# Kernel optimization log

Measured on AMD Instinct MI355X. Metric: run time of the kernel, lower is better.

Reference implementation:

```python
import jax, jax.numpy as jnp
import numpy as np
from math import factorial

# ---- static config mirroring Cace.__init__ ----
MAX_L = 3            # max angular degree
N_RBF = 8            # Bessel radial basis size
RB = 8               # n_radial_basis (radial embedding dim after transform)
K = 3                # n_atom_basis -> edge channels C = K*K
NZ = 4               # len(zs)
CUTOFF = 5.5
N_NODES = 2000
N_EDGES = 50000
T_MP = 1             # num_message_passing
MP_NORM = 1.0 / np.sqrt(25.0)   # 1/sqrt(avg_num_neighbors)
C = K * K

def _lxlylz(max_l):
    out = []
    for l in range(max_l + 1):
        for lx in range(l, -1, -1):
            for ly in range(l - lx, -1, -1):
                out.append((lx, ly, l - lx - ly))
    return out

L_LIST = _lxlylz(MAX_L)                 # 20 Cartesian monomials for max_l=3
NL = len(L_LIST)
LX = np.array([t[0] for t in L_LIST]); LY = np.array([t[1] for t in L_LIST]); LZ = np.array([t[2] for t in L_LIST])
DEGS = LX + LY + LZ                     # degree l of each monomial
MULTI = np.array([factorial(int(d)) / (factorial(int(a)) * factorial(int(b)) * factorial(int(c)))
                  for a, b, c, d in zip(LX, LY, LZ, DEGS)], dtype=np.float32)
SEL = np.zeros((NL, MAX_L + 1), np.float32)
SEL[np.arange(NL), DEGS] = 1.0          # monomial -> degree one-hot (for per-l sums)
NB = 1 + (MAX_L + 1)                    # symmetrizer feats: nu=1 (l=0) + nu=2 per l

def bessel(r):  # [E] -> [E, N_RBF]
    n = jnp.arange(1, N_RBF + 1, dtype=r.dtype)
    return jnp.sqrt(2.0 / CUTOFF) * jnp.sin(n[None, :] * jnp.pi * r[:, None] / CUTOFF) / r[:, None]

def poly_cutoff(r):  # MACE-style polynomial cutoff, p=6
    p = 6.0
    u = r / CUTOFF
    f = 1.0 - (p + 1.0) * (p + 2.0) / 2.0 * u**6 + p * (p + 2.0) * u**7 - p * (p + 1.0) / 2.0 * u**8
    return f * (u < 1.0)

def axis_pows(x):  # [E] -> [E, MAX_L+1] = x^0..x^MAX_L (safe grads, handles negatives)
    pows = [jnp.ones_like(x)]
    for _ in range(MAX_L):
        pows.append(pows[-1] * x)
    return jnp.stack(pows, axis=1)

def angular(u):  # unit vectors [E,3] -> Cartesian monomials [E, NL]
    return axis_pows(u[:, 0])[:, LX] * axis_pows(u[:, 1])[:, LY] * axis_pows(u[:, 2])[:, LZ]

def radial_transform(x, W):  # x [N,R,L,C], W [MAX_L+1,R,Rb] shared per degree l
    return jnp.einsum('nrlc,lrb->nblc', x, W[DEGS])

def symmetrize(A):  # A [N,Rb,NL,C] -> B [N,Rb,NB,C]
    b1 = A[:, :, :1, :]  # nu=1: the (0,0,0) monomial (index 0)
    w = (A * A) * jnp.asarray(MULTI)[None, None, :, None]
    b2 = jnp.einsum('nrlc,lm->nrmc', w, jnp.asarray(SEL))  # nu=2 invariant per degree l
    return jnp.concatenate([b1, b2], axis=2)


def setup_inputs() -> dict:
    key = jax.random.key(0)
    ks = jax.random.split(key, 9)
    positions = jax.random.uniform(ks[0], (N_NODES, 3), dtype=jnp.float32) * 12.0
    species = jax.random.randint(ks[1], (N_NODES,), 0, NZ)
    send = jax.random.randint(ks[2], (N_EDGES,), 0, N_NODES)
    off = jax.random.randint(ks[3], (N_EDGES,), 1, N_NODES)
    recv = (send + off) % N_NODES  # no self-edges -> strictly positive edge lengths
    edge_index = jnp.stack([send, recv])
    shifts = jnp.zeros((N_EDGES, 3), jnp.float32)
    W_embed = jax.random.normal(ks[4], (NZ, K), jnp.float32)
    W_radial = jax.random.normal(ks[5], (MAX_L + 1, N_RBF, RB), jnp.float32) / np.sqrt(N_RBF)
    W_mem = jax.random.normal(ks[6], (MAX_L + 1, RB, RB), jnp.float32) / np.sqrt(RB)
    W_ar = jax.random.normal(ks[7], (N_RBF, RB), jnp.float32) / np.sqrt(N_RBF)
    W_chi = jax.random.normal(ks[8], (RB, NB), jnp.float32) * 0.1
    return {"positions": positions, "shifts": shifts, "W_embed": W_embed, "W_radial": W_radial,
            "W_mem": W_mem, "W_ar": W_ar, "W_chi": W_chi, "species": species, "edge_index": edge_index}


def reference(positions, shifts, W_embed, W_radial, W_mem, W_ar, W_chi, species, edge_index):
    n_nodes = positions.shape[0]
    send, recv = edge_index[0], edge_index[1]
    # edge geometry
    vec = positions[recv] - positions[send] + shifts
    lengths = jnp.linalg.norm(vec, axis=-1)
    u = vec / (lengths[:, None] + 1e-9)
    rad = bessel(lengths)          # [E,R]
    fcut = poly_cutoff(lengths)    # [E]
    ang = angular(u)               # [E,NL]
    # edge type encoding: outer product of sender/receiver species embeddings
    emb = W_embed[species]         # [N,K]
    enc = (emb[send][:, :, None] * emb[recv][:, None, :]).reshape(-1, C)  # [E,C]
    # elementwise_multiply_3tensors -> [E,R,NL,C]
    edge_attri = jnp.einsum('er,el,ec->erlc', rad * fcut[:, None], ang, enc)
    A = radial_transform(jax.ops.segment_sum(edge_attri, recv, num_segments=n_nodes), W_radial)  # [N,Rb,NL,C]
    B = symmetrize(A)              # [N,Rb,NB,C]
    feats = [B]
    for _ in range(T_MP):
        mem = jnp.einsum('nrlc,lrb->nblc', A, W_mem[DEGS])        # NodeMemory
        chi = jnp.einsum('nbkc,bk->nc', B, W_chi)                  # MessageBchi node scalar
        msg_bchi = edge_attri * chi[send][:, None, None, :]
        A_bchi = radial_transform(jax.ops.segment_sum(msg_bchi, recv, num_segments=n_nodes), W_radial)
        fr = (rad @ W_ar) * fcut[:, None]                          # MessageAr radial filter [E,Rb]
        msg_ar = A[send] * fr[:, :, None, None]
        A_ar = jax.ops.segment_sum(msg_ar, recv, num_segments=n_nodes)
        A = (A_ar + A_bchi) * MP_NORM + mem
        B = symmetrize(A)
        feats.append(B)
    return jnp.stack(feats, axis=-1)   # [N,Rb,NB,C,T_MP+1]
```

## Files before the change

kernel.cpp:

```cpp
#include <hip/hip_runtime.h>
#include <hip/hip_bf16.h>


#define CUTF 5.5f
#define MPNORM 0.2f

__constant__ int   d_DEGS[20]  = {0,1,1,1,2,2,2,2,2,2,3,3,3,3,3,3,3,3,3,3};
__constant__ float d_MULTI[20] = {1,1,1,1,1,2,2,1,2,1,1,3,3,3,6,3,1,3,3,1};

__global__ __launch_bounds__(1024) void k_prep(const int* __restrict__ eidx,
                                               int* __restrict__ offs,
                                               int* __restrict__ cursor,
                                               int N, int E) {
  __shared__ int cnt[2048];
  __shared__ int part[1024];
  int t = threadIdx.x;
  cnt[t] = 0; cnt[t + 1024] = 0;
  for (int i = t; i < N; i += 1024) cursor[i] = 0;
  __syncthreads();
  const int* recv = eidx + E;
  if ((E & 3) == 0) {
    #pragma unroll 2
    for (int i = t * 4; i + 3 < E; i += 4096) {
      int4 v = *reinterpret_cast<const int4*>(recv + i);
      atomicAdd(&cnt[v.x], 1); atomicAdd(&cnt[v.y], 1);
      atomicAdd(&cnt[v.z], 1); atomicAdd(&cnt[v.w], 1);
    }
  } else {
    #pragma unroll 4
    for (int i = t; i < E; i += 1024) atomicAdd(&cnt[recv[i]], 1);
  }
  __syncthreads();
  int a = cnt[2 * t], b = cnt[2 * t + 1];
  int s = a + b;
  part[t] = s;
  __syncthreads();
  for (int d = 1; d < 1024; d <<= 1) {
    int add = (t >= d) ? part[t - d] : 0;
    __syncthreads();
    part[t] += add;
    __syncthreads();
  }
  int excl = part[t] - s;
  if (2 * t     < N) offs[2 * t]     = excl;
  if (2 * t + 1 < N) offs[2 * t + 1] = excl + a;
  if (t == 1023) offs[N] = part[1023];
}

__global__ void k_edge(const float* __restrict__ pos,
                       const float* __restrict__ shifts,
                       const float* __restrict__ Wemb,
                       const float* __restrict__ War,
                       const int* __restrict__ species,
                       const int* __restrict__ eidx,
                       const int* __restrict__ offs,
                       int* __restrict__ cursor,
                       float* __restrict__ edata,
                       int* __restrict__ esend,
                       int E) {
  __shared__ float war_s[64];
  int t = threadIdx.x;
  if (t < 64) war_s[t] = War[t];
  __syncthreads();
  int e = blockIdx.x * blockDim.x + t;
  if (e >= E) return;
  int s  = eidx[e];
  int rI = eidx[E + e];
  float vx = pos[rI*3+0] - pos[s*3+0] + shifts[e*3+0];
  float vy = pos[rI*3+1] - pos[s*3+1] + shifts[e*3+1];
  float vz = pos[rI*3+2] - pos[s*3+2] + shifts[e*3+2];
  float len = sqrtf(vx*vx + vy*vy + vz*vz);
  float inv = 1.0f / (len + 1e-9f);
  float ux = vx*inv, uy = vy*inv, uz = vz*inv;
  float uu = len * (1.0f/CUTF);
  float u2 = uu*uu, u6 = u2*u2*u2;
  float fcut = (uu < 1.0f) ? (1.0f - 28.0f*u6 + 48.0f*u6*uu - 21.0f*u6*u2) : 0.0f;
  float x = 3.14159265358979f * uu;
  float sn = sinf(x), c2 = 2.0f*cosf(x), snm1 = 0.0f;
  float pref = sqrtf(2.0f/CUTF) / (len + 1e-20f);
  float rad[8];
  float v[48];
  #pragma unroll
  for (int k = 0; k < 8; k++) {
    rad[k] = pref * sn;
    v[k]   = rad[k] * fcut;
    float nxt = c2*sn - snm1; snm1 = sn; sn = nxt;
  }
  #pragma unroll
  for (int b = 0; b < 8; b++) {
    float a = 0.0f;
    #pragma unroll
    for (int k = 0; k < 8; k++) a += rad[k] * war_s[k*8+b];
    v[8+b] = a * fcut;
  }
  float px2 = ux*ux, py2 = uy*uy, pz2 = uz*uz;
  v[16] = 1.0f; v[17] = ux;     v[18] = uy;     v[19] = uz;
  v[20] = px2;  v[21] = ux*uy;  v[22] = ux*uz;  v[23] = py2;
  v[24] = uy*uz;v[25] = pz2;
  v[26] = px2*ux; v[27] = px2*uy; v[28] = px2*uz; v[29] = ux*py2;
  v[30] = ux*uy*uz; v[31] = ux*pz2; v[32] = py2*uy; v[33] = py2*uz;
  v[34] = uy*pz2; v[35] = pz2*uz;
  int zs = species[s], zr = species[rI];
  float es0 = Wemb[zs*3+0], es1 = Wemb[zs*3+1], es2 = Wemb[zs*3+2];
  float er0 = Wemb[zr*3+0], er1 = Wemb[zr*3+1], er2 = Wemb[zr*3+2];
  v[36] = es0*er0; v[37] = es0*er1; v[38] = es0*er2;
  v[39] = es1*er0; v[40] = es1*er1; v[41] = es1*er2;
  v[42] = es2*er0; v[43] = es2*er1; v[44] = es2*er2;
  v[45] = 0.0f; v[46] = 0.0f; v[47] = 0.0f;
  int slot = atomicAdd(&cursor[rI], 1);
  int dst = offs[rI] + slot;
  float4* eb4 = reinterpret_cast<float4*>(edata + (size_t)dst * 48);
  #pragma unroll
  for (int w = 0; w < 12; w++)
    eb4[w] = make_float4(v[4*w], v[4*w+1], v[4*w+2], v[4*w+3]);
  esend[dst] = s;
}

__global__ __launch_bounds__(192) void k_nodeA(
    const float* __restrict__ edata, const int* __restrict__ offs,
    const float* __restrict__ Wrad, const float* __restrict__ Wchi,
    float* __restrict__ A, uint4* __restrict__ Abf2,
    float* __restrict__ chi, float* __restrict__ B0, int N) {
  __shared__ float wr_s[288];
  __shared__ float wchi_s[40];
  __shared__ float Bsh[360];
  int t = threadIdx.x, n = blockIdx.x;
  for (int i = t; i < 256; i += 192) { int d = i >> 6, rm = i & 63; wr_s[d*72+rm] = Wrad[i]; }
  for (int i = t; i < 40;  i += 192) wchi_s[i] = Wchi[i];
  for (int i = t; i < 360; i += 192) Bsh[i] = 0.0f;
  int l = t / 9, c = t - l*9;
  bool act = t < 180;
  int ll = act ? l : 0, cc = act ? c : 0;
  float acc[8];
  #pragma unroll
  for (int r = 0; r < 8; r++) acc[r] = 0.0f;
  int start = offs[n], end = offs[n+1];
  #pragma unroll 4
  for (int j = start; j < end; j++) {
    const float* row = edata + (size_t)j * 48;
    float p = row[16+ll] * row[36+cc];
    #pragma unroll
    for (int r = 0; r < 8; r++) acc[r] += row[r] * p;
  }
  __syncthreads();
  int deg = act ? d_DEGS[ll] : 0;
  const float* wp = &wr_s[deg*72];
  float Ab[8];
  #pragma unroll
  for (int b = 0; b < 8; b++) {
    float a = 0.0f;
    #pragma unroll
    for (int r = 0; r < 8; r++) a += acc[r] * wp[r*8+b];
    Ab[b] = a;
  }
  if (act) {
    #pragma unroll
    for (int b = 0; b < 8; b++) A[(size_t)n*1440 + t*8 + b] = Ab[b];
    unsigned int pk[4];
    #pragma unroll
    for (int bp = 0; bp < 4; bp++) {
      __hip_bfloat16 blo = __float2bfloat16(Ab[2*bp]);
      __hip_bfloat16 bhi = __float2bfloat16(Ab[2*bp+1]);
      pk[bp] = (unsigned int)(*reinterpret_cast<unsigned short*>(&blo))
             | ((unsigned int)(*reinterpret_cast<unsigned short*>(&bhi)) << 16);
    }
    uint4 q; q.x = pk[0]; q.y = pk[1]; q.z = pk[2]; q.w = pk[3];
    Abf2[(size_t)n*180 + t] = q;
    if (l == 0) {
      #pragma unroll
      for (int b = 0; b < 8; b++) Bsh[b*45 + c] = Ab[b];
    }
    float mlt = d_MULTI[ll]; int kk = 1 + deg;
    #pragma unroll
    for (int b = 0; b < 8; b++) atomicAdd(&Bsh[b*45 + kk*9 + c], mlt*Ab[b]*Ab[b]);
  }
  __syncthreads();
  if (t < 9) {
    float s = 0.0f;
    for (int b = 0; b < 8; b++)
      #pragma unroll
      for (int kq = 0; kq < 5; kq++) s += Bsh[b*45 + kq*9 + t] * wchi_s[b*5 + kq];
    chi[n*9 + t] = s;
  }
  for (int i = t; i < 360; i += 192)
    B0[(size_t)n*360 + i] = Bsh[i];
}

__global__ __launch_bounds__(192) void k_node2(
    const float* __restrict__ edata, const int* __restrict__ esend,
    const int* __restrict__ offs,
    const float* __restrict__ Wrad, const float* __restrict__ Wmem,
    const float* __restrict__ A, const uint4* __restrict__ Abf2,
    const float* __restrict__ chi, const float* __restrict__ B0,
    float* __restrict__ out, int N) {
  __shared__ float wr_s[288], wm_s[288];
  __shared__ float Bsh[360];
  int t = threadIdx.x, n = blockIdx.x;
  for (int i = t; i < 256; i += 192) {
    int d = i >> 6, rm = i & 63;
    wr_s[d*72+rm] = Wrad[i];
    wm_s[d*72+rm] = Wmem[i];
  }
  for (int i = t; i < 360; i += 192) Bsh[i] = 0.0f;
  int l = t / 9, c = t - l*9;
  bool act = t < 180;
  int ll = act ? l : 0, cc = act ? c : 0;
  int tt = act ? t : 0;
  float Sacc[8], ARacc[8];
  #pragma unroll
  for (int r = 0; r < 8; r++) { Sacc[r] = 0.0f; ARacc[r] = 0.0f; }
  int start = offs[n], end = offs[n+1];
  #pragma unroll 4
  for (int j = start; j < end; j++) {
    const float* row = edata + (size_t)j * 48;
    int snd = esend[j];
    float ch = chi[snd*9 + cc];
    float pch = row[16+ll] * row[36+cc] * ch;
    #pragma unroll
    for (int r = 0; r < 8; r++) Sacc[r] += row[r] * pch;
    const uint4 q = Abf2[(size_t)snd*180 + tt];
    float a0 = __uint_as_float(q.x << 16), a1 = __uint_as_float(q.x & 0xffff0000u);
    float a2 = __uint_as_float(q.y << 16), a3 = __uint_as_float(q.y & 0xffff0000u);
    float a4 = __uint_as_float(q.z << 16), a5 = __uint_as_float(q.z & 0xffff0000u);
    float a6 = __uint_as_float(q.w << 16), a7 = __uint_as_float(q.w & 0xffff0000u);
    ARacc[0] += a0*row[8];  ARacc[1] += a1*row[9];
    ARacc[2] += a2*row[10]; ARacc[3] += a3*row[11];
    ARacc[4] += a4*row[12]; ARacc[5] += a5*row[13];
    ARacc[6] += a6*row[14]; ARacc[7] += a7*row[15];
  }
  __syncthreads();
  if (act) {
    int deg = d_DEGS[ll];
    const float* wrp = &wr_s[deg*72];
    const float* wmp = &wm_s[deg*72];
    const float* aop = A + (size_t)n*1440 + t*8;
    float aown[8];
    #pragma unroll
    for (int r = 0; r < 8; r++) aown[r] = aop[r];
    float newA[8];
    #pragma unroll
    for (int b = 0; b < 8; b++) {
      float mem = 0.0f, ab = 0.0f;
      #pragma unroll
      for (int r = 0; r < 8; r++) { mem += aown[r]*wmp[r*8+b]; ab += Sacc[r]*wrp[r*8+b]; }
      newA[b] = (ARacc[b] + ab)*MPNORM + mem;
    }
    if (l == 0) {
      #pragma unroll
      for (int b = 0; b < 8; b++) Bsh[b*45 + c] = newA[b];
    }
    float mlt = d_MULTI[ll]; int kk = 1 + deg;
    #pragma unroll
    for (int b = 0; b < 8; b++) atomicAdd(&Bsh[b*45 + kk*9 + c], mlt*newA[b]*newA[b]);
  }
  __syncthreads();
  float2* out2 = reinterpret_cast<float2*>(out);
  for (int i = t; i < 360; i += 192) {
    float2 pk; pk.x = B0[(size_t)n*360 + i]; pk.y = Bsh[i];
    out2[(size_t)n*360 + i] = pk;
  }
}

extern "C" void kernel_launch(void* const* d_in, const int* in_sizes, int n_in,
                              void* d_out, int out_size, void* d_ws, size_t ws_size,
                              hipStream_t stream) {
  const float* pos    = (const float*)d_in[0];
  const float* shifts = (const float*)d_in[1];
  const float* Wemb   = (const float*)d_in[2];
  const float* Wrad   = (const float*)d_in[3];
  const float* Wmem   = (const float*)d_in[4];
  const float* War    = (const float*)d_in[5];
  const float* Wchi   = (const float*)d_in[6];
  const int* species = (const int*)d_in[7];
  const int* eidx    = (const int*)d_in[8];
  float* out = (float*)d_out;
  int N = in_sizes[7];
  int E = in_sizes[8] / 2;

  char* base = (char*)d_ws;
  size_t off = 0;
  float* edata = (float*)(base + off); off += (size_t)E*48*4;
  float* A     = (float*)(base + off); off += (size_t)N*1440*4;
  uint4* Abf2  = (uint4*)(base + off); off += (size_t)N*180*16;
  float* chi   = (float*)(base + off); off += (size_t)N*9*4;
  float* B0    = (float*)(base + off); off += (size_t)N*360*4;
  int* cursor  = (int*)(base + off);   off += (size_t)N*4;
  int* offs    = (int*)(base + off);   off += (((size_t)(N+1)*4) + 15) & ~(size_t)15;
  int* esend   = (int*)(base + off);   off += (size_t)E*4;

  int eb = (E + 255) / 256;
  k_prep<<<1, 1024, 0, stream>>>(eidx, offs, cursor, N, E);
  k_edge<<<eb, 256, 0, stream>>>(pos, shifts, Wemb, War, species, eidx, offs, cursor,
                                 edata, esend, E);
  k_nodeA<<<N, 192, 0, stream>>>(edata, offs, Wrad, Wchi, A, Abf2, chi, B0, N);
  k_node2<<<N, 192, 0, stream>>>(edata, esend, offs, Wrad, Wmem, A, Abf2, chi, B0, out, N);
}
```

Measured before the change: 151.8 us.

## Fuse edge feature computation into node kernels and recompute instead of materializing

Removes the separate edge kernel and its 48-float-per-edge buffer. k_prep now builds a sorted edge permutation (eorig) from the atomic ranks, and each node kernel recomputes edge features for its incoming edges in shared-memory chunks. k_node2 recomputes the first-layer A accumulation and B0 instead of reading A and B0 from global memory. This trades extra recomputation (trig, geometry) and an extra single-block scatter pass in k_prep for less global memory traffic and one fewer launch.

```diff
diff --git a/kernel.cpp b/kernel.cpp
--- a/kernel.cpp
+++ b/kernel.cpp
@@ -4,31 +4,34 @@
 
 #define CUTF 5.5f
 #define MPNORM 0.2f
+#define RSTR 52
+#define CHUNK 64
 
 __constant__ int   d_DEGS[20]  = {0,1,1,1,2,2,2,2,2,2,3,3,3,3,3,3,3,3,3,3};
 __constant__ float d_MULTI[20] = {1,1,1,1,1,2,2,1,2,1,1,3,3,3,6,3,1,3,3,1};
 
 __global__ __launch_bounds__(1024) void k_prep(const int* __restrict__ eidx,
                                                int* __restrict__ offs,
-                                               int* __restrict__ cursor,
+                                               int* __restrict__ erank,
+                                               int* __restrict__ eorig,
                                                int N, int E) {
   __shared__ int cnt[2048];
   __shared__ int part[1024];
   int t = threadIdx.x;
   cnt[t] = 0; cnt[t + 1024] = 0;
-  for (int i = t; i < N; i += 1024) cursor[i] = 0;
   __syncthreads();
   const int* recv = eidx + E;
   if ((E & 3) == 0) {
-    #pragma unroll 2
     for (int i = t * 4; i + 3 < E; i += 4096) {
       int4 v = *reinterpret_cast<const int4*>(recv + i);
-      atomicAdd(&cnt[v.x], 1); atomicAdd(&cnt[v.y], 1);
-      atomicAdd(&cnt[v.z], 1); atomicAdd(&cnt[v.w], 1);
+      int r0 = atomicAdd(&cnt[v.x], 1);
+      int r1 = atomicAdd(&cnt[v.y], 1);
+      int r2 = atomicAdd(&cnt[v.z], 1);
+      int r3 = atomicAdd(&cnt[v.w], 1);
+      *reinterpret_cast<int4*>(erank + i) = make_int4(r0, r1, r2, r3);
     }
   } else {
-    #pragma unroll 4
-    for (int i = t; i < E; i += 1024) atomicAdd(&cnt[recv[i]], 1);
+    for (int i = t; i < E; i += 1024) erank[i] = atomicAdd(&cnt[recv[i]], 1);
   }
   __syncthreads();
   int a = cnt[2 * t], b = cnt[2 * t + 1];
@@ -45,30 +48,27 @@
   if (2 * t     < N) offs[2 * t]     = excl;
   if (2 * t + 1 < N) offs[2 * t + 1] = excl + a;
   if (t == 1023) offs[N] = part[1023];
-}
-
-__global__ void k_edge(const float* __restrict__ pos,
-                       const float* __restrict__ shifts,
-                       const float* __restrict__ Wemb,
-                       const float* __restrict__ War,
-                       const int* __restrict__ species,
-                       const int* __restrict__ eidx,
-                       const int* __restrict__ offs,
-                       int* __restrict__ cursor,
-                       float* __restrict__ edata,
-                       int* __restrict__ esend,
-                       int E) {
-  __shared__ float war_s[64];
-  int t = threadIdx.x;
-  if (t < 64) war_s[t] = War[t];
-  __syncthreads();
-  int e = blockIdx.x * blockDim.x + t;
-  if (e >= E) return;
-  int s  = eidx[e];
-  int rI = eidx[E + e];
-  float vx = pos[rI*3+0] - pos[s*3+0] + shifts[e*3+0];
-  float vy = pos[rI*3+1] - pos[s*3+1] + shifts[e*3+1];
-  float vz = pos[rI*3+2] - pos[s*3+2] + shifts[e*3+2];
+  cnt[2 * t] = excl;
+  cnt[2 * t + 1] = excl + a;
+  __syncthreads();
+  for (int i = t; i < E; i += 1024) {
+    int r = recv[i];
+    eorig[cnt[r] + erank[i]] = i;
+  }
+}
+
+template <bool WANT_FR>
+__device__ __forceinline__ void edge_feats(
+    int e, int n,
+    const float* __restrict__ pos, const float* __restrict__ shifts,
+    const float* __restrict__ Wemb, const int* __restrict__ species,
+    const int* __restrict__ eidx,
+    const float* war_s, float* row, int* snd_slot) {
+  int s = eidx[e];
+  *snd_slot = s;
+  float vx = pos[n*3+0] - pos[s*3+0] + shifts[e*3+0];
+  float vy = pos[n*3+1] - pos[s*3+1] + shifts[e*3+1];
+  float vz = pos[n*3+2] - pos[s*3+2] + shifts[e*3+2];
   float len = sqrtf(vx*vx + vy*vy + vz*vz);
   float inv = 1.0f / (len + 1e-9f);
   float ux = vx*inv, uy = vy*inv, uz = vz*inv;
@@ -79,48 +79,45 @@
   float sn = sinf(x), c2 = 2.0f*cosf(x), snm1 = 0.0f;
   float pref = sqrtf(2.0f/CUTF) / (len + 1e-20f);
   float rad[8];
-  float v[48];
   #pragma unroll
   for (int k = 0; k < 8; k++) {
     rad[k] = pref * sn;
-    v[k]   = rad[k] * fcut;
+    row[k] = rad[k] * fcut;
     float nxt = c2*sn - snm1; snm1 = sn; sn = nxt;
   }
-  #pragma unroll
-  for (int b = 0; b < 8; b++) {
-    float a = 0.0f;
-    #pragma unroll
-    for (int k = 0; k < 8; k++) a += rad[k] * war_s[k*8+b];
-    v[8+b] = a * fcut;
+  if (WANT_FR) {
+    #pragma unroll
+    for (int b = 0; b < 8; b++) {
+      float a = 0.0f;
+      #pragma unroll
+      for (int k = 0; k < 8; k++) a += rad[k] * war_s[k*8+b];
+      row[8+b] = a * fcut;
+    }
   }
   float px2 = ux*ux, py2 = uy*uy, pz2 = uz*uz;
-  v[16] = 1.0f; v[17] = ux;     v[18] = uy;     v[19] = uz;
-  v[20] = px2;  v[21] = ux*uy;  v[22] = ux*uz;  v[23] = py2;
-  v[24] = uy*uz;v[25] = pz2;
-  v[26] = px2*ux; v[27] = px2*uy; v[28] = px2*uz; v[29] = ux*py2;
-  v[30] = ux*uy*uz; v[31] = ux*pz2; v[32] = py2*uy; v[33] = py2*uz;
-  v[34] = uy*pz2; v[35] = pz2*uz;
-  int zs = species[s], zr = species[rI];
+  row[16] = 1.0f;   row[17] = ux;     row[18] = uy;     row[19] = uz;
+  row[20] = px2;    row[21] = ux*uy;  row[22] = ux*uz;  row[23] = py2;
+  row[24] = uy*uz;  row[25] = pz2;
+  row[26] = px2*ux; row[27] = px2*uy; row[28] = px2*uz; row[29] = ux*py2;
+  row[30] = ux*uy*uz; row[31] = ux*pz2; row[32] = py2*uy; row[33] = py2*uz;
+  row[34] = uy*pz2; row[35] = pz2*uz;
+  int zs = species[s], zr = species[n];
   float es0 = Wemb[zs*3+0], es1 = Wemb[zs*3+1], es2 = Wemb[zs*3+2];
   float er0 = Wemb[zr*3+0], er1 = Wemb[zr*3+1], er2 = Wemb[zr*3+2];
-  v[36] = es0*er0; v[37] = es0*er1; v[38] = es0*er2;
-  v[39] = es1*er0; v[40] = es1*er1; v[41] = es1*er2;
-  v[42] = es2*er0; v[43] = es2*er1; v[44] = es2*er2;
-  v[45] = 0.0f; v[46] = 0.0f; v[47] = 0.0f;
-  int slot = atomicAdd(&cursor[rI], 1);
-  int dst = offs[rI] + slot;
-  float4* eb4 = reinterpret_cast<float4*>(edata + (size_t)dst * 48);
-  #pragma unroll
-  for (int w = 0; w < 12; w++)
-    eb4[w] = make_float4(v[4*w], v[4*w+1], v[4*w+2], v[4*w+3]);
-  esend[dst] = s;
+  row[36] = es0*er0; row[37] = es0*er1; row[38] = es0*er2;
+  row[39] = es1*er0; row[40] = es1*er1; row[41] = es1*er2;
+  row[42] = es2*er0; row[43] = es2*er1; row[44] = es2*er2;
 }
 
 __global__ __launch_bounds__(192) void k_nodeA(
-    const float* __restrict__ edata, const int* __restrict__ offs,
+    const float* __restrict__ pos, const float* __restrict__ shifts,
+    const float* __restrict__ Wemb, const int* __restrict__ species,
+    const int* __restrict__ eidx, const int* __restrict__ eorig,
+    const int* __restrict__ offs,
     const float* __restrict__ Wrad, const float* __restrict__ Wchi,
-    float* __restrict__ A, uint4* __restrict__ Abf2,
-    float* __restrict__ chi, float* __restrict__ B0, int N) {
+    uint4* __restrict__ Abf2, float* __restrict__ chi, int N) {
+  __shared__ __align__(16) float srow[CHUNK * RSTR];
+  __shared__ int ssnd[CHUNK];
   __shared__ float wr_s[288];
   __shared__ float wchi_s[40];
   __shared__ float Bsh[360];
@@ -134,17 +131,29 @@
   float acc[8];
   #pragma unroll
   for (int r = 0; r < 8; r++) acc[r] = 0.0f;
-  int start = offs[n], end = offs[n+1];
-  #pragma unroll 4
-  for (int j = start; j < end; j++) {
-    const float* row = edata + (size_t)j * 48;
-    float p = row[16+ll] * row[36+cc];
-    #pragma unroll
-    for (int r = 0; r < 8; r++) acc[r] += row[r] * p;
-  }
-  __syncthreads();
-  int deg = act ? d_DEGS[ll] : 0;
-  const float* wp = &wr_s[deg*72];
+  int start = offs[n], deg = offs[n+1] - start;
+  for (int cb = 0; cb < deg; cb += CHUNK) {
+    int cnum = min(CHUNK, deg - cb);
+    __syncthreads();
+    if (t < cnum) {
+      int e = eorig[start + cb + t];
+      edge_feats<false>(e, n, pos, shifts, Wemb, species, eidx,
+                        nullptr, &srow[t*RSTR], &ssnd[t]);
+    }
+    __syncthreads();
+    #pragma unroll 4
+    for (int j = 0; j < cnum; j++) {
+      const float* row = &srow[j*RSTR];
+      float4 g0 = *reinterpret_cast<const float4*>(row);
+      float4 g1 = *reinterpret_cast<const float4*>(row + 4);
+      float p = row[16+ll] * row[36+cc];
+      acc[0] += g0.x*p; acc[1] += g0.y*p; acc[2] += g0.z*p; acc[3] += g0.w*p;
+      acc[4] += g1.x*p; acc[5] += g1.y*p; acc[6] += g1.z*p; acc[7] += g1.w*p;
+    }
+  }
+  __syncthreads();
+  int dg = act ? d_DEGS[ll] : 0;
+  const float* wp = &wr_s[dg*72];
   float Ab[8];
   #pragma unroll
   for (int b = 0; b < 8; b++) {
@@ -154,8 +163,6 @@
     Ab[b] = a;
   }
   if (act) {
-    #pragma unroll
-    for (int b = 0; b < 8; b++) A[(size_t)n*1440 + t*8 + b] = Ab[b];
     unsigned int pk[4];
     #pragma unroll
     for (int bp = 0; bp < 4; bp++) {
@@ -164,13 +171,13 @@
       pk[bp] = (unsigned int)(*reinterpret_cast<unsigned short*>(&blo))
              | ((unsigned int)(*reinterpret_cast<unsigned short*>(&bhi)) << 16);
     }
-    uint4 q; q.x = pk[0]; q.y = pk[1]; q.z = pk[2]; q.w = pk[3];
-    Abf2[(size_t)n*180 + t] = q;
+    uint4 qv; qv.x = pk[0]; qv.y = pk[1]; qv.z = pk[2]; qv.w = pk[3];
+    Abf2[(size_t)n*180 + t] = qv;
     if (l == 0) {
       #pragma unroll
       for (int b = 0; b < 8; b++) Bsh[b*45 + c] = Ab[b];
     }
-    float mlt = d_MULTI[ll]; int kk = 1 + deg;
+    float mlt = d_MULTI[ll]; int kk = 1 + dg;
     #pragma unroll
     for (int b = 0; b < 8; b++) atomicAdd(&Bsh[b*45 + kk*9 + c], mlt*Ab[b]*Ab[b]);
   }
@@ -182,81 +189,107 @@
       for (int kq = 0; kq < 5; kq++) s += Bsh[b*45 + kq*9 + t] * wchi_s[b*5 + kq];
     chi[n*9 + t] = s;
   }
-  for (int i = t; i < 360; i += 192)
-    B0[(size_t)n*360 + i] = Bsh[i];
 }
 
 __global__ __launch_bounds__(192) void k_node2(
-    const float* __restrict__ edata, const int* __restrict__ esend,
+    const float* __restrict__ pos, const float* __restrict__ shifts,
+    const float* __restrict__ Wemb, const int* __restrict__ species,
+    const int* __restrict__ eidx, const int* __restrict__ eorig,
     const int* __restrict__ offs,
     const float* __restrict__ Wrad, const float* __restrict__ Wmem,
-    const float* __restrict__ A, const uint4* __restrict__ Abf2,
-    const float* __restrict__ chi, const float* __restrict__ B0,
+    const float* __restrict__ War,
+    const uint4* __restrict__ Abf2, const float* __restrict__ chi,
     float* __restrict__ out, int N) {
+  __shared__ __align__(16) float srow[CHUNK * RSTR];
+  __shared__ int ssnd[CHUNK];
   __shared__ float wr_s[288], wm_s[288];
-  __shared__ float Bsh[360];
+  __shared__ float war_s[64];
+  __shared__ float Bsh1[360], Bsh2[360];
   int t = threadIdx.x, n = blockIdx.x;
   for (int i = t; i < 256; i += 192) {
     int d = i >> 6, rm = i & 63;
     wr_s[d*72+rm] = Wrad[i];
     wm_s[d*72+rm] = Wmem[i];
   }
-  for (int i = t; i < 360; i += 192) Bsh[i] = 0.0f;
+  if (t < 64) war_s[t] = War[t];
+  for (int i = t; i < 360; i += 192) { Bsh1[i] = 0.0f; Bsh2[i] = 0.0f; }
   int l = t / 9, c = t - l*9;
   bool act = t < 180;
   int ll = act ? l : 0, cc = act ? c : 0;
   int tt = act ? t : 0;
-  float Sacc[8], ARacc[8];
+  float acc[8], Sacc[8], ARacc[8];
   #pragma unroll
-  for (int r = 0; r < 8; r++) { Sacc[r] = 0.0f; ARacc[r] = 0.0f; }
-  int start = offs[n], end = offs[n+1];
-  #pragma unroll 4
-  for (int j = start; j < end; j++) {
-    const float* row = edata + (size_t)j * 48;
-    int snd = esend[j];
-    float ch = chi[snd*9 + cc];
-    float pch = row[16+ll] * row[36+cc] * ch;
-    #pragma unroll
-    for (int r = 0; r < 8; r++) Sacc[r] += row[r] * pch;
-    const uint4 q = Abf2[(size_t)snd*180 + tt];
-    float a0 = __uint_as_float(q.x << 16), a1 = __uint_as_float(q.x & 0xffff0000u);
-    float a2 = __uint_as_float(q.y << 16), a3 = __uint_as_float(q.y & 0xffff0000u);
-    float a4 = __uint_as_float(q.z << 16), a5 = __uint_as_float(q.z & 0xffff0000u);
-    float a6 = __uint_as_float(q.w << 16), a7 = __uint_as_float(q.w & 0xffff0000u);
-    ARacc[0] += a0*row[8];  ARacc[1] += a1*row[9];
-    ARacc[2] += a2*row[10]; ARacc[3] += a3*row[11];
-    ARacc[4] += a4*row[12]; ARacc[5] += a5*row[13];
-    ARacc[6] += a6*row[14]; ARacc[7] += a7*row[15];
+  for (int r = 0; r < 8; r++) { acc[r] = 0.0f; Sacc[r] = 0.0f; ARacc[r] = 0.0f; }
+  int start = offs[n], deg = offs[n+1] - start;
+  for (int cb = 0; cb < deg; cb += CHUNK) {
+    int cnum = min(CHUNK, deg - cb);
+    __syncthreads();
+    if (t < cnum) {
+      int e = eorig[start + cb + t];
+      edge_feats<true>(e, n, pos, shifts, Wemb, species, eidx,
+                       war_s, &srow[t*RSTR], &ssnd[t]);
+    }
+    __syncthreads();
+    #pragma unroll 2
+    for (int j = 0; j < cnum; j++) {
+      const float* row = &srow[j*RSTR];
+      int snd = ssnd[j];
+      float ch = chi[snd*9 + cc];
+      const uint4 qv = Abf2[(size_t)snd*180 + tt];
+      float4 g0 = *reinterpret_cast<const float4*>(row);
+      float4 g1 = *reinterpret_cast<const float4*>(row + 4);
+      float4 f0 = *reinterpret_cast<const float4*>(row + 8);
+      float4 f1 = *reinterpret_cast<const float4*>(row + 12);
+      float p = row[16+ll] * row[36+cc];
+      float pch = p * ch;
+      acc[0] += g0.x*p;  acc[1] += g0.y*p;  acc[2] += g0.z*p;  acc[3] += g0.w*p;
+      acc[4] += g1.x*p;  acc[5] += g1.y*p;  acc[6] += g1.z*p;  acc[7] += g1.w*p;
+      Sacc[0] += g0.x*pch; Sacc[1] += g0.y*pch; Sacc[2] += g0.z*pch; Sacc[3] += g0.w*pch;
+      Sacc[4] += g1.x*pch; Sacc[5] += g1.y*pch; Sacc[6] += g1.z*pch; Sacc[7] += g1.w*pch;
+      float a0 = __uint_as_float(qv.x << 16), a1 = __uint_as_float(qv.x & 0xffff0000u);
+      float a2 = __uint_as_float(qv.y << 16), a3 = __uint_as_float(qv.y & 0xffff0000u);
+      float a4 = __uint_as_float(qv.z << 16), a5 = __uint_as_float(qv.z & 0xffff0000u);
+      float a6 = __uint_as_float(qv.w << 16), a7 = __uint_as_float(qv.w & 0xffff0000u);
+      ARacc[0] += a0*f0.x; ARacc[1] += a1*f0.y; ARacc[2] += a2*f0.z; ARacc[3] += a3*f0.w;
+      ARacc[4] += a4*f1.x; ARacc[5] += a5*f1.y; ARacc[6] += a6*f1.z; ARacc[7] += a7*f1.w;
+    }
   }
   __syncthreads();
   if (act) {
-    int deg = d_DEGS[ll];
-    const float* wrp = &wr_s[deg*72];
-    const float* wmp = &wm_s[deg*72];
-    const float* aop = A + (size_t)n*1440 + t*8;
-    float aown[8];
-    #pragma unroll
-    for (int r = 0; r < 8; r++) aown[r] = aop[r];
+    int dg = d_DEGS[ll];
+    float mlt = d_MULTI[ll]; int kk = 1 + dg;
+    const float* wrp = &wr_s[dg*72];
+    const float* wmp = &wm_s[dg*72];
+    float Ab[8];
+    #pragma unroll
+    for (int b = 0; b < 8; b++) {
+      float a = 0.0f;
+      #pragma unroll
+      for (int r = 0; r < 8; r++) a += acc[r] * wrp[r*8+b];
+      Ab[b] = a;
+    }
     float newA[8];
     #pragma unroll
     for (int b = 0; b < 8; b++) {
       float mem = 0.0f, ab = 0.0f;
       #pragma unroll
-      for (int r = 0; r < 8; r++) { mem += aown[r]*wmp[r*8+b]; ab += Sacc[r]*wrp[r*8+b]; }
+      for (int r = 0; r < 8; r++) { mem += Ab[r]*wmp[r*8+b]; ab += Sacc[r]*wrp[r*8+b]; }
       newA[b] = (ARacc[b] + ab)*MPNORM + mem;
     }
     if (l == 0) {
       #pragma unroll
-      for (int b = 0; b < 8; b++) Bsh[b*45 + c] = newA[b];
-    }
-    float mlt = d_MULTI[ll]; int kk = 1 + deg;
-    #pragma unroll
-    for (int b = 0; b < 8; b++) atomicAdd(&Bsh[b*45 + kk*9 + c], mlt*newA[b]*newA[b]);
+      for (int b = 0; b < 8; b++) { Bsh1[b*45 + c] = Ab[b]; Bsh2[b*45 + c] = newA[b]; }
+    }
+    #pragma unroll
+    for (int b = 0; b < 8; b++) {
+      atomicAdd(&Bsh1[b*45 + kk*9 + c], mlt*Ab[b]*Ab[b]);
+      atomicAdd(&Bsh2[b*45 + kk*9 + c], mlt*newA[b]*newA[b]);
+    }
   }
   __syncthreads();
   float2* out2 = reinterpret_cast<float2*>(out);
   for (int i = t; i < 360; i += 192) {
-    float2 pk; pk.x = B0[(size_t)n*360 + i]; pk.y = Bsh[i];
+    float2 pk; pk.x = Bsh1[i]; pk.y = Bsh2[i];
     out2[(size_t)n*360 + i] = pk;
   }
 }
@@ -279,19 +312,15 @@
 
   char* base = (char*)d_ws;
   size_t off = 0;
-  float* edata = (float*)(base + off); off += (size_t)E*48*4;
-  float* A     = (float*)(base + off); off += (size_t)N*1440*4;
   uint4* Abf2  = (uint4*)(base + off); off += (size_t)N*180*16;
   float* chi   = (float*)(base + off); off += (size_t)N*9*4;
-  float* B0    = (float*)(base + off); off += (size_t)N*360*4;
-  int* cursor  = (int*)(base + off);   off += (size_t)N*4;
   int* offs    = (int*)(base + off);   off += (((size_t)(N+1)*4) + 15) & ~(size_t)15;
-  int* esend   = (int*)(base + off);   off += (size_t)E*4;
-
-  int eb = (E + 255) / 256;
-  k_prep<<<1, 1024, 0, stream>>>(eidx, offs, cursor, N, E);
-  k_edge<<<eb, 256, 0, stream>>>(pos, shifts, Wemb, War, species, eidx, offs, cursor,
-                                 edata, esend, E);
-  k_nodeA<<<N, 192, 0, stream>>>(edata, offs, Wrad, Wchi, A, Abf2, chi, B0, N);
-  k_node2<<<N, 192, 0, stream>>>(edata, esend, offs, Wrad, Wmem, A, Abf2, chi, B0, out, N);
-}
+  int* erank   = (int*)(base + off);   off += (((size_t)E*4) + 15) & ~(size_t)15;
+  int* eorig   = (int*)(base + off);   off += (((size_t)E*4) + 15) & ~(size_t)15;
+
+  k_prep<<<1, 1024, 0, stream>>>(eidx, offs, erank, eorig, N, E);
+  k_nodeA<<<N, 192, 0, stream>>>(pos, shifts, Wemb, species, eidx, eorig, offs,
+                                 Wrad, Wchi, Abf2, chi, N);
+  k_node2<<<N, 192, 0, stream>>>(pos, shifts, Wemb, species, eidx, eorig, offs,
+                                 Wrad, Wmem, War, Abf2, chi, out, N);
+}
```

New measurement: 205.4 us. +35.3%, slower.
